# Performance work log

Hardware: AMD Instinct MI355X
Metric: run time of the kernel (lower is better)

The kernel has to match this reference:

```python
import jax, jax.numpy as jnp
import numpy as np

B, N, DIM = 1, 4096, 1024
HEADS, DIM_HEAD = 12, 8
POST_LOG_SCALE = 1.0
SCALE = DIM_HEAD ** -0.5


def setup_inputs() -> dict:
    key = jax.random.key(0)
    kx, kw = jax.random.split(key)
    x = jax.random.normal(kx, (B, N, DIM), dtype=jnp.float32)
    # torch nn.Linear(dim, heads*dim_head*2, bias=False) weight: [2*heads*dim_head, dim]
    W = jax.random.normal(kw, (2 * HEADS * DIM_HEAD, DIM), dtype=jnp.float32) * (DIM ** -0.5)
    return {"x": x, "W": W}


def reference(x, W):
    b, n, _ = x.shape
    # linear: x @ W^T -> [b, n, 2*h*d]; rearrange '(qk h d) -> qk b h n d'
    proj = jnp.einsum('bnc,oc->bno', x, W)
    proj = proj.reshape(b, n, 2, HEADS, DIM_HEAD)
    q = jnp.transpose(proj[:, :, 0], (0, 2, 1, 3))  # [b, h, n, d]
    k = jnp.transpose(proj[:, :, 1], (0, 2, 1, 3))  # [b, h, n, d]
    # small-d QK matmul -> [b, h, n, n]
    gates = jnp.einsum('bhid,bhjd->bhij', q, k) * SCALE
    gates = jax.nn.log_sigmoid(gates) * POST_LOG_SCALE
    # causal_mask = triu(ones, diagonal=0); masked_fill -> zero on/above diagonal
    i = jnp.arange(n)[:, None]
    j = jnp.arange(n)[None, :]
    keep = j < i  # strictly lower-triangular entries survive
    gates = jnp.where(keep, gates, 0.0)
    # flip-cumsum-flip == reverse cumulative sum along last axis
    gates = jax.lax.cumsum(gates, axis=3, reverse=True)
    return gates
```

## Files before the change

### kernel.cpp

```cpp
#include <hip/hip_runtime.h>

#define NTOK 4096
#define DIMC 1024
#define HEADS 12
#define DH 8
#define QSCALE 0.35355339059327373f
#define LOG2E  1.4426950408889634f
#define LN2    0.6931471805599453f
#define QPRE   (QSCALE * LOG2E)

typedef float f4 __attribute__((ext_vector_type(4)));
typedef float f2 __attribute__((ext_vector_type(2)));

#define KOFF (HEADS * NTOK * DH)

__global__ __launch_bounds__(256) void k1_proj(const float* __restrict__ x,
                                               const float* __restrict__ W,
                                               float* __restrict__ qk) {
    __shared__ float xs[8 * 1028];
    const int t = threadIdx.x;
    const int row0 = blockIdx.x * 8;

    const f4* x4 = (const f4*)(x + (size_t)row0 * DIMC);
    #pragma unroll
    for (int i = 0; i < 8; ++i) {
        int f = t + i * 256;
        int r = f >> 8;
        int c4 = f & 255;
        f4 v = x4[f];
        *(f4*)(&xs[r * 1028 + c4 * 4]) = v;
    }
    __syncthreads();

    const int g  = t >> 2;
    const int rg = t & 3;

    f2 acc[2][3];
    #pragma unroll
    for (int a = 0; a < 2; ++a)
        #pragma unroll
        for (int m = 0; m < 3; ++m) acc[a][m] = (f2)(0.f);

    const float* w0 = W + (size_t)(3 * g) * DIMC;
    #pragma unroll 2
    for (int c = 0; c < DIMC; c += 4) {
        f4 w[3];
        #pragma unroll
        for (int m = 0; m < 3; ++m)
            w[m] = *(const f4*)(w0 + (size_t)m * DIMC + c);
        #pragma unroll
        for (int a = 0; a < 2; ++a) {
            f4 xv = *(const f4*)(&xs[(rg * 2 + a) * 1028 + c]);
            #pragma unroll
            for (int m = 0; m < 3; ++m) {
                acc[a][m] = __builtin_elementwise_fma(xv.xy, w[m].xy, acc[a][m]);
                acc[a][m] = __builtin_elementwise_fma(xv.zw, w[m].zw, acc[a][m]);
            }
        }
    }

    #pragma unroll
    for (int m = 0; m < 3; ++m) {
        int o   = 3 * g + m;
        int qkf = (o >= 96) ? 1 : 0;
        int oo  = o - 96 * qkf;
        int h   = oo >> 3;
        int d   = oo & 7;
        #pragma unroll
        for (int a = 0; a < 2; ++a) {
            int n = row0 + rg * 2 + a;
            float v = acc[a][m].x + acc[a][m].y;
            if (!qkf) {
                qk[((size_t)h * NTOK + n) * DH + d] = v * QPRE;
            } else {
                qk[KOFF + (((size_t)h * 16 + (n >> 8)) * DH + d) * 256 + (n & 255)] = v;
            }
        }
    }
}

__device__ __forceinline__ float lsig2(float u) {
    float mn = fminf(u, 0.f);
    float z  = __builtin_amdgcn_exp2f(-fabsf(u));
    return mn - __builtin_amdgcn_logf(1.f + z);
}

__global__ __launch_bounds__(512) void k2_gates(const float* __restrict__ qk,
                                                float* __restrict__ out) {
    const int bid  = blockIdx.x;
    const int h    = bid >> 9;
    const int i0   = (bid & 511) << 3;
    const int t    = threadIdx.x;
    const int lane = t & 63;
    const int wid  = t >> 6;
    const int r    = i0 + wid;

    const float* qp = qk + ((size_t)h * NTOK + r) * DH;
    float q[8];
    #pragma unroll
    for (int d = 0; d < 8; ++d) q[d] = qp[d];

    const float* kh = qk + KOFF + (size_t)h * (16 * DH * 256) + 4 * lane;
    float* o = out + ((size_t)h * NTOK + r) * NTOK;

    const int cb = r >> 8;
    const int bb = cb >> 2;

    const f4 z = (f4)(0.f);

    for (int b = 3; b > bb; --b) {
        float* ob = o + b * 1024 + 4 * lane;
        #pragma unroll
        for (int sub = 0; sub < 4; ++sub)
            __builtin_nontemporal_store(z, (f4*)(ob + sub * 256));
    }

    float carry = 0.f;
    for (int b = bb; b >= 0; --b) {
        f4 ov[4];
        #pragma unroll
        for (int sub = 3; sub >= 0; --sub) {
            const int cc = b * 4 + sub;
            if (cc > cb) { ov[sub] = z; continue; }

            const float* kc = kh + (size_t)cc * 2048;
            f4 kv[8];
            #pragma unroll
            for (int d = 0; d < 8; ++d) kv[d] = *(const f4*)(kc + d * 256);

            f2 A = (f2)(0.f), B = (f2)(0.f);
            #pragma unroll
            for (int d = 0; d < 8; ++d) {
                A = __builtin_elementwise_fma(kv[d].xy, (f2)(q[d]), A);
                B = __builtin_elementwise_fma(kv[d].zw, (f2)(q[d]), B);
            }

            const int j0 = cc * 256 + 4 * lane;
            float g0, g1, g2, g3;
            if (cc == cb) {
                g0 = (j0 + 0 < r) ? lsig2(A.x) : 0.f;
                g1 = (j0 + 1 < r) ? lsig2(A.y) : 0.f;
                g2 = (j0 + 2 < r) ? lsig2(B.x) : 0.f;
                g3 = (j0 + 3 < r) ? lsig2(B.y) : 0.f;
            } else {
                g0 = lsig2(A.x); g1 = lsig2(A.y);
                g2 = lsig2(B.x); g3 = lsig2(B.y);
            }

            g2 += g3; g1 += g2; g0 += g1;
            const float tot = g0;
            float s = tot;
            #pragma unroll
            for (int off = 1; off < 64; off <<= 1) {
                float v = __shfl_down(s, off, 64);
                if (lane + off < 64) s += v;
            }
            const float base = (s - tot) + carry;
            carry += __builtin_amdgcn_readfirstlane(s);

            f4 gv = {g0, g1, g2, g3};
            ov[sub] = (gv + base) * LN2;
        }

        float* ob = o + b * 1024 + 4 * lane;
        #pragma unroll
        for (int sub = 0; sub < 4; ++sub)
            __builtin_nontemporal_store(ov[sub], (f4*)(ob + sub * 256));
    }
}

extern "C" void kernel_launch(void* const* d_in, const int* in_sizes, int n_in,
                              void* d_out, int out_size, void* d_ws, size_t ws_size,
                              hipStream_t stream) {
    const float* x = (const float*)d_in[0];
    const float* W = (const float*)d_in[1];
    float* out = (float*)d_out;
    float* qk  = (float*)d_ws;

    hipLaunchKernelGGL(k1_proj, dim3(NTOK / 8), dim3(256), 0, stream, x, W, qk);
    hipLaunchKernelGGL(k2_gates, dim3(HEADS * NTOK / 8), dim3(512), 0, stream, qk, out);
}
```

Measured before the change: 204.1 us.

## Split each gate row across eight waves with shared-memory cross-wave scan

```diff
diff --git a/kernel.cpp b/kernel.cpp
--- a/kernel.cpp
+++ b/kernel.cpp
@@ -88,12 +88,13 @@
 __global__ __launch_bounds__(512) void k2_gates(const float* __restrict__ qk,
                                                 float* __restrict__ out) {
     const int bid  = blockIdx.x;
-    const int h    = bid >> 9;
-    const int i0   = (bid & 511) << 3;
+    const int h    = bid >> 12;
+    const int r    = bid & (NTOK - 1);
     const int t    = threadIdx.x;
     const int lane = t & 63;
     const int wid  = t >> 6;
-    const int r    = i0 + wid;
+
+    __shared__ float wt[2][8];
 
     const float* qp = qk + ((size_t)h * NTOK + r) * DH;
     float q[8];
@@ -102,27 +103,21 @@
 
     const float* kh = qk + KOFF + (size_t)h * (16 * DH * 256) + 4 * lane;
     float* o = out + ((size_t)h * NTOK + r) * NTOK;
-
     const int cb = r >> 8;
-    const int bb = cb >> 2;
 
     const f4 z = (f4)(0.f);
+    float carry = 0.f;
 
-    for (int b = 3; b > bb; --b) {
-        float* ob = o + b * 1024 + 4 * lane;
-        #pragma unroll
-        for (int sub = 0; sub < 4; ++sub)
-            __builtin_nontemporal_store(z, (f4*)(ob + sub * 256));
-    }
+    #pragma unroll
+    for (int half = 1; half >= 0; --half) {
+        const int cc = half * 8 + wid;
+        const int j0 = cc * 256 + 4 * lane;
+        const bool live = (cc <= cb);
 
-    float carry = 0.f;
-    for (int b = bb; b >= 0; --b) {
-        f4 ov[4];
-        #pragma unroll
-        for (int sub = 3; sub >= 0; --sub) {
-            const int cc = b * 4 + sub;
-            if (cc > cb) { ov[sub] = z; continue; }
+        f4 gv = z;
+        float tot = 0.f, s = 0.f, wtotal = 0.f;
 
+        if (live) {
             const float* kc = kh + (size_t)cc * 2048;
             f4 kv[8];
             #pragma unroll
@@ -135,7 +130,6 @@
                 B = __builtin_elementwise_fma(kv[d].zw, (f2)(q[d]), B);
             }
 
-            const int j0 = cc * 256 + 4 * lane;
             float g0, g1, g2, g3;
             if (cc == cb) {
                 g0 = (j0 + 0 < r) ? lsig2(A.x) : 0.f;
@@ -148,24 +142,31 @@
             }
 
             g2 += g3; g1 += g2; g0 += g1;
-            const float tot = g0;
-            float s = tot;
+            tot = g0;
+            s = tot;
             #pragma unroll
             for (int off = 1; off < 64; off <<= 1) {
                 float v = __shfl_down(s, off, 64);
                 if (lane + off < 64) s += v;
             }
-            const float base = (s - tot) + carry;
-            carry += __builtin_amdgcn_readfirstlane(s);
-
-            f4 gv = {g0, g1, g2, g3};
-            ov[sub] = (gv + base) * LN2;
+            wtotal = __builtin_amdgcn_readfirstlane(s);
+            gv.x = g0; gv.y = g1; gv.z = g2; gv.w = g3;
         }
 
-        float* ob = o + b * 1024 + 4 * lane;
+        if (lane == 0) wt[half][wid] = live ? wtotal : 0.f;
+        __syncthreads();
+
+        float ib = carry, tot8 = 0.f;
         #pragma unroll
-        for (int sub = 0; sub < 4; ++sub)
-            __builtin_nontemporal_store(ov[sub], (f4*)(ob + sub * 256));
+        for (int w2 = 0; w2 < 8; ++w2) {
+            float v = wt[half][w2];
+            tot8 += v;
+            if (w2 > wid) ib += v;
+        }
+        carry += tot8;
+
+        f4 ov = live ? ((gv + ((s - tot) + ib)) * LN2) : z;
+        __builtin_nontemporal_store(ov, (f4*)(o + j0));
     }
 }
 
@@ -178,5 +179,5 @@
     float* qk  = (float*)d_ws;
 
     hipLaunchKernelGGL(k1_proj, dim3(NTOK / 8), dim3(256), 0, stream, x, W, qk);
-    hipLaunchKernelGGL(k2_gates, dim3(HEADS * NTOK / 8), dim3(512), 0, stream, qk, out);
+    hipLaunchKernelGGL(k2_gates, dim3(HEADS * NTOK), dim3(512), 0, stream, qk, out);
 }
```

Measured after the change: 221.7 us. 1.09x slower.
